# Performance work log

Hardware: AMD Instinct MI355X
Metric: run time of the kernel (lower is better)

Reference implementation:

```python
import jax, jax.numpy as jnp
import numpy as np

B, N, D, H = 2, 2048, 1024, 16
DK = D // H
SCALE = DK ** -0.5


def setup_inputs() -> dict:
    key = jax.random.key(0)
    ks = jax.random.split(key, 11)
    s = D ** -0.5
    return {
        "q": jax.random.normal(ks[0], (B, N, D), jnp.float32),
        "k": jax.random.normal(ks[1], (B, N, D), jnp.float32),
        "v": jax.random.normal(ks[2], (B, N, D), jnp.float32),
        "Wq": jax.random.normal(ks[3], (D, D), jnp.float32) * s,
        "bq": jnp.zeros((D,), jnp.float32),
        "Wk": jax.random.normal(ks[4], (D, D), jnp.float32) * s,
        "bk": jnp.zeros((D,), jnp.float32),
        "Wv": jax.random.normal(ks[5], (D, D), jnp.float32) * s,
        "bv": jnp.zeros((D,), jnp.float32),
        "Wo": jax.random.normal(ks[6], (D, D), jnp.float32) * s,
        "bo": jnp.zeros((D,), jnp.float32),
    }


def _split_heads(x):
    # [b, n, h*d] -> [b, h, n, d]
    b, n, _ = x.shape
    return x.reshape(b, n, H, DK).transpose(0, 2, 1, 3)


def reference(q, k, v, Wq, bq, Wk, bk, Wv, bv, Wo, bo):
    qh = _split_heads(q @ Wq.T + bq)
    kh = _split_heads(k @ Wk.T + bk)
    vh = _split_heads(v @ Wv.T + bv)
    dots = jnp.einsum('bhid,bhjd->bhij', qh, kh) * SCALE
    attn = jax.nn.softmax(dots, axis=-1)
    out = jnp.einsum('bhij,bhjd->bhid', attn, vh)
    out = out.transpose(0, 2, 1, 3).reshape(q.shape[0], q.shape[1], D)
    return out @ Wo.T + bo
```

## Files before the change

### kernel.cpp

```cpp
#include <hip/hip_runtime.h>
#include <hip/hip_bf16.h>
#include <cstdint>
#include <cstddef>

#define BB 2
#define NN 2048
#define DD 1024
#define HH 16
#define DKK 64
#define SCALE 0.125f
#define LOG2E 1.4426950408889634f

typedef __bf16 bf16;
typedef __bf16 bf16x4 __attribute__((ext_vector_type(4)));
typedef __bf16 bf16x8 __attribute__((ext_vector_type(8)));
typedef float f32x4 __attribute__((ext_vector_type(4)));
typedef short s16x4 __attribute__((ext_vector_type(4)));

#define GLD(gp, lp)                                                            \
  __builtin_amdgcn_global_load_lds(                                            \
      (const __attribute__((address_space(1))) void*)(gp),                     \
      (__attribute__((address_space(3))) void*)(lp), 16, 0, 0)

struct CvtArgs { const float* s[7]; bf16* d[7]; int n[7]; };

__global__ void k_cvt(CvtArgs a) {
  const int seg = blockIdx.y;
  const float* __restrict__ s = a.s[seg];
  bf16* __restrict__ d = a.d[seg];
  int i = (blockIdx.x * 256 + threadIdx.x) * 8;
  if (i >= a.n[seg]) return;
  float4 f0 = *(const float4*)(s + i);
  float4 f1 = *(const float4*)(s + i + 4);
  bf16x8 o;
  o[0] = (bf16)f0.x; o[1] = (bf16)f0.y; o[2] = (bf16)f0.z; o[3] = (bf16)f0.w;
  o[4] = (bf16)f1.x; o[5] = (bf16)f1.y; o[6] = (bf16)f1.z; o[7] = (bf16)f1.w;
  *(bf16x8*)(d + i) = o;
}

__device__ __forceinline__ void gemm_body(
    const bf16* __restrict__ A, const bf16* __restrict__ W,
    const float* __restrict__ bias, bf16* __restrict__ outB,
    float* __restrict__ outF, int mode, float oscale, int m0, int n0) {
  const int K = 1024;
  __shared__ bf16 lA[128 * 64];
  __shared__ bf16 lB[128 * 64];
  const int t = threadIdx.x;
  const int lane = t & 63, quad = lane >> 4, l16 = lane & 15, w = t >> 6;
  const int wm = (w >> 1) * 64, wn = (w & 1) * 64;

  f32x4 acc[4][4] = {};

  const bf16* gA[4]; const bf16* gB[4];
#pragma unroll
  for (int i4 = 0; i4 < 4; i4++) {
    int i = i4 * 256 + t;
    int r = i >> 3, c = (i & 7) ^ (r & 7);
    gA[i4] = A + (size_t)(m0 + r) * K + c * 8;
    gB[i4] = W + (size_t)(n0 + r) * K + c * 8;
  }

  for (int kb = 0; kb < K; kb += 64) {
    __syncthreads();
#pragma unroll
    for (int i4 = 0; i4 < 4; i4++) {
      GLD(gA[i4] + kb, lA + (i4 * 256 + t) * 8);
      GLD(gB[i4] + kb, lB + (i4 * 256 + t) * 8);
    }
    __syncthreads();

#pragma unroll
    for (int kb2 = 0; kb2 < 2; kb2++) {
      bf16x8 af[4], bfr[4];
#pragma unroll
      for (int i = 0; i < 4; i++) {
        int ch = ((kb2 * 4 + quad) ^ (l16 & 7)) * 8;
        af[i] = *(const bf16x8*)(lA + (wm + i * 16 + l16) * 64 + ch);
        bfr[i] = *(const bf16x8*)(lB + (wn + i * 16 + l16) * 64 + ch);
      }
#pragma unroll
      for (int mi = 0; mi < 4; mi++)
#pragma unroll
        for (int ni = 0; ni < 4; ni++)
          acc[mi][ni] = __builtin_amdgcn_mfma_f32_16x16x32_bf16(
              af[mi], bfr[ni], acc[mi][ni], 0, 0, 0);
    }
  }

#pragma unroll
  for (int mi = 0; mi < 4; mi++) {
#pragma unroll
    for (int ni = 0; ni < 4; ni++) {
#pragma unroll
      for (int r = 0; r < 4; r++) {
        int gm = m0 + wm + mi * 16 + quad * 4 + r;
        int gn = n0 + wn + ni * 16 + l16;
        float v = (acc[mi][ni][r] + bias[gn]) * oscale;
        if (mode == 3) {
          outF[(size_t)gm * 1024 + gn] = v;
        } else {
          int b = gm >> 11, row = gm & 2047;
          int h = gn >> 6, dk = gn & 63;
          if (mode == 2)
            outB[((size_t)(b * HH + h) * DKK + dk) * NN + row] = (bf16)v;
          else
            outB[((size_t)(b * HH + h) * NN + row) * DKK + dk] = (bf16)v;
        }
      }
    }
  }
}

struct QkvArgs {
  const bf16* A; const bf16* W; const float* b[3]; bf16* o[3]; float sc0;
};

__global__ __launch_bounds__(256, 3) void k_qkv(QkvArgs g) {
  const int z = blockIdx.z;
  gemm_body(g.A + (size_t)z * 4194304, g.W + (size_t)z * 1048576, g.b[z],
            g.o[z], nullptr, z == 2 ? 2 : 0, z == 0 ? g.sc0 : 1.0f,
            blockIdx.y * 128, blockIdx.x * 128);
}

__global__ __launch_bounds__(256, 3) void k_oproj(
    const bf16* __restrict__ A, const bf16* __restrict__ W,
    const float* __restrict__ bias, float* __restrict__ out) {
  gemm_body(A, W, bias, nullptr, out, 3, 1.0f, blockIdx.y * 128,
            blockIdx.x * 128);
}

__global__ __launch_bounds__(256, 2) void k_attn(
    const bf16* __restrict__ Qp, const bf16* __restrict__ Kp,
    const bf16* __restrict__ Vt, bf16* __restrict__ Ao) {
  __shared__ bf16 lK[2][128 * 64];
  __shared__ bf16 lV[2][64 * 128];
  const int t = threadIdx.x;
  const int lane = t & 63, quad = lane >> 4, l16 = lane & 15, w = t >> 6;
  const int bh = blockIdx.x;
  const int qt = blockIdx.y;
  const bf16* Qb = Qp + (size_t)bh * NN * DKK;
  const bf16* Kb = Kp + (size_t)bh * NN * DKK;
  const bf16* Vb = Vt + (size_t)bh * DKK * NN;

  const int qr0 = qt * 128 + w * 32;
  bf16x8 qf[2][2];
#pragma unroll
  for (int j = 0; j < 2; j++)
#pragma unroll
    for (int kq = 0; kq < 2; kq++)
      qf[j][kq] = *(const bf16x8*)(Qb + (size_t)(qr0 + j * 16 + l16) * DKK +
                                   kq * 32 + quad * 8);

  float lj[2] = {0.f, 0.f};
  f32x4 oaccT[2][4] = {};

  const bf16* gK[4]; const bf16* gV[4];
#pragma unroll
  for (int i4 = 0; i4 < 4; i4++) {
    int i = i4 * 256 + t;
    int rK = i >> 3, cK = (i & 7) ^ (rK & 7);
    gK[i4] = Kb + (size_t)rK * DKK + cK * 8;
    int rV = i >> 4, cV = (i & 15) ^ (rV & 15);
    gV[i4] = Vb + (size_t)rV * NN + cV * 8;
  }
  const int swzK0 = (quad ^ (l16 & 7)) * 8;
  const int swzK1 = ((4 + quad) ^ (l16 & 7)) * 8;

#pragma unroll
  for (int i4 = 0; i4 < 4; i4++) {
    GLD(gK[i4], &lK[0][(i4 * 256 + t) * 8]);
    GLD(gV[i4], &lV[0][(i4 * 256 + t) * 8]);
  }

  int p = 0;
  for (int kt = 0; kt < NN; kt += 128) {
    __syncthreads();
    if (kt + 128 < NN) {
#pragma unroll
      for (int i4 = 0; i4 < 4; i4++) {
        GLD(gK[i4] + (size_t)(kt + 128) * DKK, &lK[p ^ 1][(i4 * 256 + t) * 8]);
        GLD(gV[i4] + (kt + 128), &lV[p ^ 1][(i4 * 256 + t) * 8]);
      }
    }

    f32x4 s[2][8];
#pragma unroll
    for (int tt = 0; tt < 8; tt++) {
      const bf16* kbase = &lK[p][(tt * 16 + l16) * 64];
      bf16x8 kf0 = *(const bf16x8*)(kbase + swzK0);
      bf16x8 kf1 = *(const bf16x8*)(kbase + swzK1);
#pragma unroll
      for (int j = 0; j < 2; j++) {
        f32x4 z = {0.f, 0.f, 0.f, 0.f};
        z = __builtin_amdgcn_mfma_f32_16x16x32_bf16(kf0, qf[j][0], z, 0, 0, 0);
        z = __builtin_amdgcn_mfma_f32_16x16x32_bf16(kf1, qf[j][1], z, 0, 0, 0);
        s[j][tt] = z;
      }
    }

    s16x4 pa[2][8];
#pragma unroll
    for (int j = 0; j < 2; j++) {
      float rs = 0.f;
#pragma unroll
      for (int tt = 0; tt < 8; tt++) {
        bf16x4 pb;
#pragma unroll
        for (int r = 0; r < 4; r++) {
          float pe = __builtin_amdgcn_exp2f(s[j][tt][r]);
          rs += pe;
          pb[r] = (bf16)pe;
        }
        pa[j][tt] = __builtin_bit_cast(s16x4, pb);
      }
      lj[j] += rs;
    }

#pragma unroll
    for (int tt = 0; tt < 8; tt++) {
#pragma unroll
      for (int ni = 0; ni < 4; ni++) {
        int rv = ni * 16 + l16;
        int cc = 2 * tt + (quad >> 1);
        const bf16* vaddr =
            &lV[p][rv * 128 + ((cc ^ l16) * 8) + (quad & 1) * 4];
        s16x4 vb = __builtin_bit_cast(s16x4, *(const bf16x4*)vaddr);
#pragma unroll
        for (int j = 0; j < 2; j++)
          oaccT[j][ni] = __builtin_amdgcn_mfma_f32_16x16x16bf16_1k(
              vb, pa[j][tt], oaccT[j][ni], 0, 0, 0);
      }
    }
    p ^= 1;
  }

  const int b = bh >> 4, h = bh & 15;
#pragma unroll
  for (int j = 0; j < 2; j++) {
    float l = lj[j];
    l += __shfl_xor(l, 16);
    l += __shfl_xor(l, 32);
    const float inv = 1.0f / l;
    bf16* dst = Ao + ((size_t)(b * NN) + qr0 + j * 16 + l16) * DD + h * DKK +
                quad * 4;
#pragma unroll
    for (int ni = 0; ni < 4; ni++) {
      bf16x4 ov;
#pragma unroll
      for (int r = 0; r < 4; r++) ov[r] = (bf16)(oaccT[j][ni][r] * inv);
      *(bf16x4*)(dst + ni * 16) = ov;
    }
  }
}

extern "C" void kernel_launch(void* const* d_in, const int* in_sizes, int n_in,
                              void* d_out, int out_size, void* d_ws,
                              size_t ws_size, hipStream_t stream) {
  const float* qin = (const float*)d_in[0];
  const float* kin = (const float*)d_in[1];
  const float* vin = (const float*)d_in[2];
  const float* Wq = (const float*)d_in[3];
  const float* bq = (const float*)d_in[4];
  const float* Wk = (const float*)d_in[5];
  const float* bk = (const float*)d_in[6];
  const float* Wv = (const float*)d_in[7];
  const float* bv = (const float*)d_in[8];
  const float* Wo = (const float*)d_in[9];
  const float* bo = (const float*)d_in[10];
  float* out = (float*)d_out;

  const int MN = BB * NN * DD;
  const int WNel = DD * DD;
  bf16* ws = (bf16*)d_ws;
  bf16* Xb = ws;
  bf16* Wb = Xb + 3 * MN;
  bf16* Qp = Wb + 4 * WNel;
  bf16* Kp = Qp + MN;
  bf16* Vt = Kp + MN;
  bf16* Ao = Xb;

  CvtArgs ca{{qin, kin, vin, Wq, Wk, Wv, Wo},
             {Xb, Xb + MN, Xb + 2 * MN, Wb, Wb + WNel, Wb + 2 * WNel,
              Wb + 3 * WNel},
             {MN, MN, MN, WNel, WNel, WNel, WNel}};
  k_cvt<<<dim3(2048, 7), 256, 0, stream>>>(ca);

  QkvArgs g{Xb, Wb, {bq, bk, bv}, {Qp, Kp, Vt}, SCALE * LOG2E};
  k_qkv<<<dim3(8, 32, 3), 256, 0, stream>>>(g);
  k_attn<<<dim3(32, 16), 256, 0, stream>>>(Qp, Kp, Vt, Ao);
  k_oproj<<<dim3(8, 32), 256, 0, stream>>>(Ao, Wb + 3 * WNel, bo, out);
}
```

Measured before the change: 225.4 us.

## Use 8 waves per attention block and narrower output-projection tiles

The attention kernel moves from 4 waves handling 32 query rows each to 8 waves handling 16 rows each, with the same 128-row tile. This halves per-wave registers and lets more waves share each K/V LDS tile. The output projection GEMM is templated to a 64-column N tile, doubling its grid from 256 to 512 blocks to fill the CUs better. Launch bounds rise for all kernels. The trade-off is more LDS reads per MFMA in attention, since K and V fragments are reused across one row block instead of two.

```diff
diff --git a/kernel.cpp b/kernel.cpp
--- a/kernel.cpp
+++ b/kernel.cpp
@@ -38,50 +38,58 @@
   *(bf16x8*)(d + i) = o;
 }
 
+template <int BN>
 __device__ __forceinline__ void gemm_body(
     const bf16* __restrict__ A, const bf16* __restrict__ W,
     const float* __restrict__ bias, bf16* __restrict__ outB,
     float* __restrict__ outF, int mode, float oscale, int m0, int n0) {
   const int K = 1024;
+  constexpr int NI = BN / 32;
+  constexpr int BI = BN * 8 / 256;
   __shared__ bf16 lA[128 * 64];
-  __shared__ bf16 lB[128 * 64];
+  __shared__ bf16 lB[BN * 64];
   const int t = threadIdx.x;
   const int lane = t & 63, quad = lane >> 4, l16 = lane & 15, w = t >> 6;
-  const int wm = (w >> 1) * 64, wn = (w & 1) * 64;
-
-  f32x4 acc[4][4] = {};
-
-  const bf16* gA[4]; const bf16* gB[4];
+  const int wm = (w >> 1) * 64, wn = (w & 1) * (BN / 2);
+
+  f32x4 acc[4][NI] = {};
+
+  const bf16* gA[4]; const bf16* gB[BI];
 #pragma unroll
   for (int i4 = 0; i4 < 4; i4++) {
     int i = i4 * 256 + t;
     int r = i >> 3, c = (i & 7) ^ (r & 7);
     gA[i4] = A + (size_t)(m0 + r) * K + c * 8;
+  }
+#pragma unroll
+  for (int i4 = 0; i4 < BI; i4++) {
+    int i = i4 * 256 + t;
+    int r = i >> 3, c = (i & 7) ^ (r & 7);
     gB[i4] = W + (size_t)(n0 + r) * K + c * 8;
   }
 
   for (int kb = 0; kb < K; kb += 64) {
     __syncthreads();
 #pragma unroll
-    for (int i4 = 0; i4 < 4; i4++) {
-      GLD(gA[i4] + kb, lA + (i4 * 256 + t) * 8);
-      GLD(gB[i4] + kb, lB + (i4 * 256 + t) * 8);
-    }
+    for (int i4 = 0; i4 < 4; i4++) GLD(gA[i4] + kb, lA + (i4 * 256 + t) * 8);
+#pragma unroll
+    for (int i4 = 0; i4 < BI; i4++) GLD(gB[i4] + kb, lB + (i4 * 256 + t) * 8);
     __syncthreads();
 
 #pragma unroll
     for (int kb2 = 0; kb2 < 2; kb2++) {
-      bf16x8 af[4], bfr[4];
-#pragma unroll
-      for (int i = 0; i < 4; i++) {
-        int ch = ((kb2 * 4 + quad) ^ (l16 & 7)) * 8;
+      bf16x8 af[4], bfr[NI];
+      const int ch = ((kb2 * 4 + quad) ^ (l16 & 7)) * 8;
+#pragma unroll
+      for (int i = 0; i < 4; i++)
         af[i] = *(const bf16x8*)(lA + (wm + i * 16 + l16) * 64 + ch);
+#pragma unroll
+      for (int i = 0; i < NI; i++)
         bfr[i] = *(const bf16x8*)(lB + (wn + i * 16 + l16) * 64 + ch);
-      }
 #pragma unroll
       for (int mi = 0; mi < 4; mi++)
 #pragma unroll
-        for (int ni = 0; ni < 4; ni++)
+        for (int ni = 0; ni < NI; ni++)
           acc[mi][ni] = __builtin_amdgcn_mfma_f32_16x16x32_bf16(
               af[mi], bfr[ni], acc[mi][ni], 0, 0, 0);
     }
@@ -90,7 +98,7 @@
 #pragma unroll
   for (int mi = 0; mi < 4; mi++) {
 #pragma unroll
-    for (int ni = 0; ni < 4; ni++) {
+    for (int ni = 0; ni < NI; ni++) {
 #pragma unroll
       for (int r = 0; r < 4; r++) {
         int gm = m0 + wm + mi * 16 + quad * 4 + r;
@@ -115,21 +123,21 @@
   const bf16* A; const bf16* W; const float* b[3]; bf16* o[3]; float sc0;
 };
 
-__global__ __launch_bounds__(256, 3) void k_qkv(QkvArgs g) {
+__global__ __launch_bounds__(256, 4) void k_qkv(QkvArgs g) {
   const int z = blockIdx.z;
-  gemm_body(g.A + (size_t)z * 4194304, g.W + (size_t)z * 1048576, g.b[z],
-            g.o[z], nullptr, z == 2 ? 2 : 0, z == 0 ? g.sc0 : 1.0f,
-            blockIdx.y * 128, blockIdx.x * 128);
-}
-
-__global__ __launch_bounds__(256, 3) void k_oproj(
+  gemm_body<128>(g.A + (size_t)z * 4194304, g.W + (size_t)z * 1048576,
+                 g.b[z], g.o[z], nullptr, z == 2 ? 2 : 0,
+                 z == 0 ? g.sc0 : 1.0f, blockIdx.y * 128, blockIdx.x * 128);
+}
+
+__global__ __launch_bounds__(256, 4) void k_oproj(
     const bf16* __restrict__ A, const bf16* __restrict__ W,
     const float* __restrict__ bias, float* __restrict__ out) {
-  gemm_body(A, W, bias, nullptr, out, 3, 1.0f, blockIdx.y * 128,
-            blockIdx.x * 128);
-}
-
-__global__ __launch_bounds__(256, 2) void k_attn(
+  gemm_body<64>(A, W, bias, nullptr, out, 3, 1.0f, blockIdx.y * 128,
+                blockIdx.x * 64);
+}
+
+__global__ __launch_bounds__(512, 4) void k_attn(
     const bf16* __restrict__ Qp, const bf16* __restrict__ Kp,
     const bf16* __restrict__ Vt, bf16* __restrict__ Ao) {
   __shared__ bf16 lK[2][128 * 64];
@@ -142,34 +150,32 @@
   const bf16* Kb = Kp + (size_t)bh * NN * DKK;
   const bf16* Vb = Vt + (size_t)bh * DKK * NN;
 
-  const int qr0 = qt * 128 + w * 32;
-  bf16x8 qf[2][2];
-#pragma unroll
-  for (int j = 0; j < 2; j++)
-#pragma unroll
-    for (int kq = 0; kq < 2; kq++)
-      qf[j][kq] = *(const bf16x8*)(Qb + (size_t)(qr0 + j * 16 + l16) * DKK +
-                                   kq * 32 + quad * 8);
-
-  float lj[2] = {0.f, 0.f};
-  f32x4 oaccT[2][4] = {};
-
-  const bf16* gK[4]; const bf16* gV[4];
-#pragma unroll
-  for (int i4 = 0; i4 < 4; i4++) {
-    int i = i4 * 256 + t;
+  const int qr0 = qt * 128 + w * 16;
+  bf16x8 qf[2];
+#pragma unroll
+  for (int kq = 0; kq < 2; kq++)
+    qf[kq] = *(const bf16x8*)(Qb + (size_t)(qr0 + l16) * DKK + kq * 32 +
+                              quad * 8);
+
+  float lj = 0.f;
+  f32x4 oaccT[4] = {};
+
+  const bf16* gK[2]; const bf16* gV[2];
+#pragma unroll
+  for (int i2 = 0; i2 < 2; i2++) {
+    int i = i2 * 512 + t;
     int rK = i >> 3, cK = (i & 7) ^ (rK & 7);
-    gK[i4] = Kb + (size_t)rK * DKK + cK * 8;
+    gK[i2] = Kb + (size_t)rK * DKK + cK * 8;
     int rV = i >> 4, cV = (i & 15) ^ (rV & 15);
-    gV[i4] = Vb + (size_t)rV * NN + cV * 8;
+    gV[i2] = Vb + (size_t)rV * NN + cV * 8;
   }
   const int swzK0 = (quad ^ (l16 & 7)) * 8;
   const int swzK1 = ((4 + quad) ^ (l16 & 7)) * 8;
 
 #pragma unroll
-  for (int i4 = 0; i4 < 4; i4++) {
-    GLD(gK[i4], &lK[0][(i4 * 256 + t) * 8]);
-    GLD(gV[i4], &lV[0][(i4 * 256 + t) * 8]);
+  for (int i2 = 0; i2 < 2; i2++) {
+    GLD(gK[i2], &lK[0][(i2 * 512 + t) * 8]);
+    GLD(gV[i2], &lV[0][(i2 * 512 + t) * 8]);
   }
 
   int p = 0;
@@ -177,44 +183,38 @@
     __syncthreads();
     if (kt + 128 < NN) {
 #pragma unroll
-      for (int i4 = 0; i4 < 4; i4++) {
-        GLD(gK[i4] + (size_t)(kt + 128) * DKK, &lK[p ^ 1][(i4 * 256 + t) * 8]);
-        GLD(gV[i4] + (kt + 128), &lV[p ^ 1][(i4 * 256 + t) * 8]);
-      }
-    }
-
-    f32x4 s[2][8];
+      for (int i2 = 0; i2 < 2; i2++) {
+        GLD(gK[i2] + (size_t)(kt + 128) * DKK, &lK[p ^ 1][(i2 * 512 + t) * 8]);
+        GLD(gV[i2] + (kt + 128), &lV[p ^ 1][(i2 * 512 + t) * 8]);
+      }
+    }
+
+    f32x4 s[8];
 #pragma unroll
     for (int tt = 0; tt < 8; tt++) {
       const bf16* kbase = &lK[p][(tt * 16 + l16) * 64];
       bf16x8 kf0 = *(const bf16x8*)(kbase + swzK0);
       bf16x8 kf1 = *(const bf16x8*)(kbase + swzK1);
-#pragma unroll
-      for (int j = 0; j < 2; j++) {
-        f32x4 z = {0.f, 0.f, 0.f, 0.f};
-        z = __builtin_amdgcn_mfma_f32_16x16x32_bf16(kf0, qf[j][0], z, 0, 0, 0);
-        z = __builtin_amdgcn_mfma_f32_16x16x32_bf16(kf1, qf[j][1], z, 0, 0, 0);
-        s[j][tt] = z;
-      }
-    }
-
-    s16x4 pa[2][8];
-#pragma unroll
-    for (int j = 0; j < 2; j++) {
-      float rs = 0.f;
-#pragma unroll
-      for (int tt = 0; tt < 8; tt++) {
-        bf16x4 pb;
-#pragma unroll
-        for (int r = 0; r < 4; r++) {
-          float pe = __builtin_amdgcn_exp2f(s[j][tt][r]);
-          rs += pe;
-          pb[r] = (bf16)pe;
-        }
-        pa[j][tt] = __builtin_bit_cast(s16x4, pb);
-      }
-      lj[j] += rs;
-    }
+      f32x4 z = {0.f, 0.f, 0.f, 0.f};
+      z = __builtin_amdgcn_mfma_f32_16x16x32_bf16(kf0, qf[0], z, 0, 0, 0);
+      z = __builtin_amdgcn_mfma_f32_16x16x32_bf16(kf1, qf[1], z, 0, 0, 0);
+      s[tt] = z;
+    }
+
+    s16x4 pa[8];
+    float rs = 0.f;
+#pragma unroll
+    for (int tt = 0; tt < 8; tt++) {
+      bf16x4 pb;
+#pragma unroll
+      for (int r = 0; r < 4; r++) {
+        float pe = __builtin_amdgcn_exp2f(s[tt][r]);
+        rs += pe;
+        pb[r] = (bf16)pe;
+      }
+      pa[tt] = __builtin_bit_cast(s16x4, pb);
+    }
+    lj += rs;
 
 #pragma unroll
     for (int tt = 0; tt < 8; tt++) {
@@ -225,31 +225,24 @@
         const bf16* vaddr =
             &lV[p][rv * 128 + ((cc ^ l16) * 8) + (quad & 1) * 4];
         s16x4 vb = __builtin_bit_cast(s16x4, *(const bf16x4*)vaddr);
-#pragma unroll
-        for (int j = 0; j < 2; j++)
-          oaccT[j][ni] = __builtin_amdgcn_mfma_f32_16x16x16bf16_1k(
-              vb, pa[j][tt], oaccT[j][ni], 0, 0, 0);
+        oaccT[ni] = __builtin_amdgcn_mfma_f32_16x16x16bf16_1k(vb, pa[tt],
+                                                              oaccT[ni], 0, 0, 0);
       }
     }
     p ^= 1;
   }
 
+  lj += __shfl_xor(lj, 16);
+  lj += __shfl_xor(lj, 32);
+  const float inv = 1.0f / lj;
   const int b = bh >> 4, h = bh & 15;
-#pragma unroll
-  for (int j = 0; j < 2; j++) {
-    float l = lj[j];
-    l += __shfl_xor(l, 16);
-    l += __shfl_xor(l, 32);
-    const float inv = 1.0f / l;
-    bf16* dst = Ao + ((size_t)(b * NN) + qr0 + j * 16 + l16) * DD + h * DKK +
-                quad * 4;
-#pragma unroll
-    for (int ni = 0; ni < 4; ni++) {
-      bf16x4 ov;
-#pragma unroll
-      for (int r = 0; r < 4; r++) ov[r] = (bf16)(oaccT[j][ni][r] * inv);
-      *(bf16x4*)(dst + ni * 16) = ov;
-    }
+  bf16* dst = Ao + ((size_t)(b * NN) + qr0 + l16) * DD + h * DKK + quad * 4;
+#pragma unroll
+  for (int ni = 0; ni < 4; ni++) {
+    bf16x4 ov;
+#pragma unroll
+    for (int r = 0; r < 4; r++) ov[r] = (bf16)(oaccT[ni][r] * inv);
+    *(bf16x4*)(dst + ni * 16) = ov;
   }
 }
 
@@ -287,6 +280,6 @@
 
   QkvArgs g{Xb, Wb, {bq, bk, bv}, {Qp, Kp, Vt}, SCALE * LOG2E};
   k_qkv<<<dim3(8, 32, 3), 256, 0, stream>>>(g);
-  k_attn<<<dim3(32, 16), 256, 0, stream>>>(Qp, Kp, Vt, Ao);
-  k_oproj<<<dim3(8, 32), 256, 0, stream>>>(Ao, Wb + 3 * WNel, bo, out);
-}
+  k_attn<<<dim3(32, 16), 512, 0, stream>>>(Qp, Kp, Vt, Ao);
+  k_oproj<<<dim3(16, 32), 256, 0, stream>>>(Ao, Wb + 3 * WNel, bo, out);
+}
```

Result: slower. 249.5 us (+10.7%).
